# Kernel tuning notes

Hardware: AMD Instinct MI355X
Metric: run time of the kernel (lower is better)

## Reference

```python
import jax, jax.numpy as jnp
import numpy as np

B, T, N, F_IN, F_OUT = 8, 64, 256, 128, 64
NEG_INF = -9e15


def setup_inputs() -> dict:
    key = jax.random.key(0)
    k_h, k_w, k_a, k_adj = jax.random.split(key, 4)
    h = jax.random.normal(k_h, (B, T, N, F_IN), dtype=jnp.float32)
    W = jax.random.normal(k_w, (F_IN, F_OUT), dtype=jnp.float32) * (1.414 / np.sqrt(F_IN))
    a = jax.random.normal(k_a, (2 * F_OUT, 1), dtype=jnp.float32) * 0.1
    # binary adjacency with guaranteed self-loops so every softmax row is valid
    adj = (jax.random.uniform(k_adj, (N, N)) > 0.5).astype(jnp.float32)
    adj = jnp.maximum(adj, jnp.eye(N, dtype=jnp.float32))
    return {"h": h, "W": W, "a": a, "adj": adj}


def reference(h, W, a, adj):
    # Wh: [B, T, N, F_OUT]
    Wh = jnp.einsum('btnf,fo->btno', h, W)
    a1 = a[:F_OUT, 0]   # [F_OUT]
    a2 = a[F_OUT:, 0]   # [F_OUT]
    Wh1 = jnp.einsum('btno,o->btn', Wh, a1)  # source scores
    Wh2 = jnp.einsum('btno,o->btn', Wh, a2)  # target scores
    # e: [B, T, N, N] = leakyrelu(Wh1_i + Wh2_j)
    e = jax.nn.leaky_relu(Wh1[..., :, None] + Wh2[..., None, :], negative_slope=0.01)
    attention = jnp.where(adj > 0, e, NEG_INF)
    alpha = jax.nn.softmax(attention, axis=-1)
    # dropout is identity at inference (training=False)
    h_prime = jnp.einsum('btnm,btmo->btno', alpha, Wh)
    return jax.nn.elu(h_prime)  # concat=True path
```

## Files before the change

### kernel.cpp

```cpp
#include <hip/hip_runtime.h>
#include <hip/hip_bf16.h>

#define NN 256
#define FI 128
#define FO 64
#define LOG2E 1.4426950408889634f

typedef short s16x8 __attribute__((ext_vector_type(8)));
typedef float f32x4 __attribute__((ext_vector_type(4)));

__device__ __forceinline__ unsigned f2bf1(float x) {
  union { float f; unsigned u; } v; v.f = x;
  unsigned r = v.u + 0x7FFFu + ((v.u >> 16) & 1u);
  return r >> 16;
}
__device__ __forceinline__ unsigned pack2(float a, float b) {
  return f2bf1(a) | (f2bf1(b) << 16);
}
__device__ __forceinline__ unsigned pktrunc(float lo, float hi) {
  union { float f; unsigned u; } a, b; a.f = hi; b.f = lo;
  return __builtin_amdgcn_perm(a.u, b.u, 0x07060302u);
}
__device__ __forceinline__ float fexp2(float x) {
#if __has_builtin(__builtin_amdgcn_exp2f)
  return __builtin_amdgcn_exp2f(x);
#else
  return exp2f(x);
#endif
}

__device__ __forceinline__ void gload_lds16(const void* g, void* l) {
#if __has_builtin(__builtin_amdgcn_global_load_lds)
  __builtin_amdgcn_global_load_lds(
      (const __attribute__((address_space(1))) unsigned*)g,
      (__attribute__((address_space(3))) unsigned*)l, 16, 0, 0);
#else
  *(uint4*)l = *(const uint4*)g;
#endif
}

__global__ __launch_bounds__(256, 4)
void gat_wh(const float* __restrict__ h, const float* __restrict__ W,
            const float* __restrict__ a,
            unsigned short* __restrict__ whG,
            float* __restrict__ wh1G, float* __restrict__ wh2G)
{
  const int bid  = blockIdx.x;
  const int g    = bid >> 2;
  const int qt   = bid & 3;
  const int tid  = threadIdx.x;
  const int lane = tid & 63;
  const int w2   = tid >> 6;
  const int m    = lane & 15;
  const int q    = lane >> 4;
  const int R    = 64 * qt + 16 * w2;

  __shared__ __align__(16) unsigned short sWT[64 * 136];

  const float* __restrict__ hB = h + (size_t)g * NN * FI;

  float4 x[4][2];
  #pragma unroll
  for (int kt = 0; kt < 4; ++kt) {
    const float* p = hB + (size_t)(R + m) * FI + kt * 32 + q * 8;
    x[kt][0] = *(const float4*)p;
    x[kt][1] = *(const float4*)(p + 4);
  }

  #pragma unroll
  for (int it = 0; it < 4; ++it) {
    int idx = it * 256 + tid;
    int k   = (idx >> 4) << 1;
    int o   = (idx & 15) << 2;
    float4 wa = *(const float4*)&W[k * FO + o];
    float4 wb = *(const float4*)&W[(k + 1) * FO + o];
    *(unsigned*)&sWT[(o + 0) * 136 + k] = pack2(wa.x, wb.x);
    *(unsigned*)&sWT[(o + 1) * 136 + k] = pack2(wa.y, wb.y);
    *(unsigned*)&sWT[(o + 2) * 136 + k] = pack2(wa.z, wb.z);
    *(unsigned*)&sWT[(o + 3) * 136 + k] = pack2(wa.w, wb.w);
  }

  float a1v[4], a2v[4];
  #pragma unroll
  for (int nt = 0; nt < 4; ++nt) {
    a1v[nt] = a[16 * nt + m];
    a2v[nt] = a[FO + 16 * nt + m];
  }

  s16x8 af[4];
  #pragma unroll
  for (int kt = 0; kt < 4; ++kt) {
    union { unsigned u[4]; s16x8 v; } pk;
    pk.u[0] = pack2(x[kt][0].x, x[kt][0].y);
    pk.u[1] = pack2(x[kt][0].z, x[kt][0].w);
    pk.u[2] = pack2(x[kt][1].x, x[kt][1].y);
    pk.u[3] = pack2(x[kt][1].z, x[kt][1].w);
    af[kt] = pk.v;
  }

  __syncthreads();

  f32x4 acc[4];
  #pragma unroll
  for (int nt = 0; nt < 4; ++nt) acc[nt] = (f32x4){0.f, 0.f, 0.f, 0.f};
  #pragma unroll
  for (int kt = 0; kt < 4; ++kt)
    #pragma unroll
    for (int nt = 0; nt < 4; ++nt) {
      s16x8 bf = *(const s16x8*)&sWT[(16 * nt + m) * 136 + kt * 32 + q * 8];
      acc[nt] = __builtin_amdgcn_mfma_f32_16x16x32_bf16(af[kt], bf, acc[nt], 0, 0, 0);
    }

  {
    float p1[4] = {0.f,0.f,0.f,0.f}, p2[4] = {0.f,0.f,0.f,0.f};
    #pragma unroll
    for (int nt = 0; nt < 4; ++nt) {
      #pragma unroll
      for (int r = 0; r < 4; ++r) { p1[r] += acc[nt][r] * a1v[nt]; p2[r] += acc[nt][r] * a2v[nt]; }
    }
    #pragma unroll
    for (int off = 1; off < 16; off <<= 1)
      #pragma unroll
      for (int r = 0; r < 4; ++r) {
        p1[r] += __shfl_xor(p1[r], off);
        p2[r] += __shfl_xor(p2[r], off);
      }
    if (m == 0) {
      *(float4*)&wh1G[g * NN + R + 4 * q] =
          make_float4(p1[0]*LOG2E, p1[1]*LOG2E, p1[2]*LOG2E, p1[3]*LOG2E);
      *(float4*)&wh2G[g * NN + R + 4 * q] =
          make_float4(p2[0]*LOG2E, p2[1]*LOG2E, p2[2]*LOG2E, p2[3]*LOG2E);
    }
  }

  {
    const int Wv  = R >> 5;
    const int S   = (R >> 4) & 1;
    const int qB  = (2 * S + (q >> 1)) & 3;
    const int swz = (m & 3) ^ ((m >> 2) & 3);
    unsigned short* whP = whG + (size_t)g * (NN * FO);
    #pragma unroll
    for (int nt = 0; nt < 4; ++nt) {
      int chunk = ((Wv * 4 + nt) * 16 + m) * 4 + (qB ^ swz);
      uint2 wrv;
      wrv.x = pack2(acc[nt][0], acc[nt][1]);
      wrv.y = pack2(acc[nt][2], acc[nt][3]);
      *(uint2*)((char*)whP + chunk * 16 + (q & 1) * 8) = wrv;
    }
  }
}

__global__ __launch_bounds__(512)
__attribute__((amdgpu_waves_per_eu(4, 8)))
void gat_attn(const unsigned short* __restrict__ whG,
              const float* __restrict__ wh1G, const float* __restrict__ wh2G,
              const float* __restrict__ adj, float* __restrict__ out)
{
  const int bid  = blockIdx.x;
  const int g    = bid >> 1;
  const int hf   = bid & 1;
  const int tid  = threadIdx.x;
  const int lane = tid & 63;
  const int w2   = tid >> 6;
  const int m    = lane & 15;
  const int q    = lane >> 4;
  const int row  = 128 * hf + 16 * w2 + m;

  __shared__ __align__(16) unsigned short sWh[NN * FO];

  const unsigned short* __restrict__ whP = whG + (size_t)g * (NN * FO);
  const float* __restrict__ wh2B = wh2G + g * NN;
  const float* __restrict__ adjR = adj + (size_t)row * NN;

  #pragma unroll
  for (int i = 0; i < 4; ++i) {
    int c = i * 512 + tid;
    gload_lds16(whP + (size_t)c * 8, &sWh[(size_t)c * 8]);
  }

  const float w1 = wh1G[g * NN + row];

  s16x8 A[8];
  float sum = 0.f;
  #pragma unroll
  for (int kt = 0; kt < 8; ++kt) {
    if (kt) __builtin_amdgcn_sched_barrier(0x7);
    int j0 = kt * 32 + q * 8;
    float4 w20 = *(const float4*)&wh2B[j0];
    float4 w21 = *(const float4*)&wh2B[j0 + 4];
    float4 ad0 = *(const float4*)&adjR[j0];
    float4 ad1 = *(const float4*)&adjR[j0 + 4];
    float p[8];
    const float w2e[8] = {w20.x, w20.y, w20.z, w20.w, w21.x, w21.y, w21.z, w21.w};
    const float ade[8] = {ad0.x, ad0.y, ad0.z, ad0.w, ad1.x, ad1.y, ad1.z, ad1.w};
    #pragma unroll
    for (int e = 0; e < 8; ++e) {
      float l = w1 + w2e[e];
      l = fmaxf(l, 0.01f * l);
      float pe = fexp2(l) * ade[e];
      p[e] = pe;
      sum += pe;
    }
    union { unsigned u[4]; s16x8 v; } pk;
    pk.u[0] = pktrunc(p[0], p[1]);
    pk.u[1] = pktrunc(p[2], p[3]);
    pk.u[2] = pktrunc(p[4], p[5]);
    pk.u[3] = pktrunc(p[6], p[7]);
    A[kt] = pk.v;
  }
  sum += __shfl_xor(sum, 16);
  sum += __shfl_xor(sum, 32);
  const float inv = __builtin_amdgcn_rcpf(sum);

  __syncthreads();

  const int swz = (m & 3) ^ ((m >> 2) & 3);
  f32x4 acc[4];
  #pragma unroll
  for (int ot = 0; ot < 4; ++ot) acc[ot] = (f32x4){0.f, 0.f, 0.f, 0.f};
  #pragma unroll
  for (int kt = 0; kt < 8; ++kt) {
    #pragma unroll
    for (int ot = 0; ot < 4; ++ot) {
      int chunk = ((kt * 4 + ot) * 16 + m) * 4 + (q ^ swz);
      s16x8 whf = *(const s16x8*)&sWh[chunk * 8];
      acc[ot] = __builtin_amdgcn_mfma_f32_16x16x32_bf16(whf, A[kt], acc[ot], 0, 0, 0);
    }
  }

  float* outB = out + (size_t)g * NN * FO;
  #pragma unroll
  for (int ot = 0; ot < 4; ++ot) {
    float4 v4;
    float* vp = (float*)&v4;
    #pragma unroll
    for (int r = 0; r < 4; ++r) {
      float v = acc[ot][r] * inv;
      float ev = fexp2(v * LOG2E) - 1.f;
      vp[r] = v > 0.f ? v : ev;
    }
    *(float4*)&outB[row * FO + 16 * ot + 4 * q] = v4;
  }
}

extern "C" void kernel_launch(void* const* d_in, const int* in_sizes, int n_in,
                              void* d_out, int out_size, void* d_ws, size_t ws_size,
                              hipStream_t stream) {
  const float* h   = (const float*)d_in[0];
  const float* W   = (const float*)d_in[1];
  const float* a   = (const float*)d_in[2];
  const float* adj = (const float*)d_in[3];
  float* out = (float*)d_out;

  char* ws = (char*)d_ws;
  float*           wh1G = (float*)(ws);
  float*           wh2G = (float*)(ws + 524288);
  unsigned short*  whG  = (unsigned short*)(ws + 2 * 524288);

  gat_wh  <<<dim3(2048), dim3(256), 0, stream>>>(h, W, a, whG, wh1G, wh2G);
  gat_attn<<<dim3(1024), dim3(512), 0, stream>>>(whG, wh1G, wh2G, adj, out);
}
```

Baseline: 134.2 us.

## Compress adjacency to bitmask and process full graph per attention block

Adds a small kernel that ballots the float adjacency into a 256x256 bitmask, and the attention kernel now reads the bitmask instead of float adjacency rows, masking exp values with bit ops. Each attention block now handles all 256 rows of one graph (two row tiles per wave) instead of half, so the Wh tile is loaded into LDS once per graph rather than twice. This reduces adjacency and Wh traffic at the cost of an extra launch, half as many blocks, and more serial work per wave. The bitmask masking treats any adj>0 as 1 instead of multiplying by the adj value, which matches the reference for binary adjacency.

Measured after the change: 159.9 us. +19.2%, slower.

```diff
diff --git a/kernel.cpp b/kernel.cpp
--- a/kernel.cpp
+++ b/kernel.cpp
@@ -37,6 +37,18 @@
 #else
   *(uint4*)l = *(const uint4*)g;
 #endif
+}
+
+__global__ __launch_bounds__(256) void gat_k0(const float* __restrict__ adj,
+                                              unsigned* __restrict__ msk) {
+  const int row = blockIdx.x;
+  const int wv = threadIdx.x >> 6, lane = threadIdx.x & 63;
+  float v = adj[row * NN + wv * 64 + lane];
+  unsigned long long b = __ballot(v > 0.f);
+  if (lane == 0) {
+    msk[row * 8 + wv * 2]     = (unsigned)b;
+    msk[row * 8 + wv * 2 + 1] = (unsigned)(b >> 32);
+  }
 }
 
 __global__ __launch_bounds__(256, 4)
@@ -154,23 +166,20 @@
 __attribute__((amdgpu_waves_per_eu(4, 8)))
 void gat_attn(const unsigned short* __restrict__ whG,
               const float* __restrict__ wh1G, const float* __restrict__ wh2G,
-              const float* __restrict__ adj, float* __restrict__ out)
+              const unsigned* __restrict__ msk, float* __restrict__ out)
 {
-  const int bid  = blockIdx.x;
-  const int g    = bid >> 1;
-  const int hf   = bid & 1;
+  const int g    = blockIdx.x;
   const int tid  = threadIdx.x;
   const int lane = tid & 63;
   const int w2   = tid >> 6;
   const int m    = lane & 15;
   const int q    = lane >> 4;
-  const int row  = 128 * hf + 16 * w2 + m;
 
   __shared__ __align__(16) unsigned short sWh[NN * FO];
 
   const unsigned short* __restrict__ whP = whG + (size_t)g * (NN * FO);
   const float* __restrict__ wh2B = wh2G + g * NN;
-  const float* __restrict__ adjR = adj + (size_t)row * NN;
+  float* outB = out + (size_t)g * NN * FO;
 
   #pragma unroll
   for (int i = 0; i < 4; ++i) {
@@ -178,68 +187,74 @@
     gload_lds16(whP + (size_t)c * 8, &sWh[(size_t)c * 8]);
   }
 
-  const float w1 = wh1G[g * NN + row];
-
-  s16x8 A[8];
-  float sum = 0.f;
-  #pragma unroll
-  for (int kt = 0; kt < 8; ++kt) {
-    if (kt) __builtin_amdgcn_sched_barrier(0x7);
-    int j0 = kt * 32 + q * 8;
-    float4 w20 = *(const float4*)&wh2B[j0];
-    float4 w21 = *(const float4*)&wh2B[j0 + 4];
-    float4 ad0 = *(const float4*)&adjR[j0];
-    float4 ad1 = *(const float4*)&adjR[j0 + 4];
-    float p[8];
-    const float w2e[8] = {w20.x, w20.y, w20.z, w20.w, w21.x, w21.y, w21.z, w21.w};
-    const float ade[8] = {ad0.x, ad0.y, ad0.z, ad0.w, ad1.x, ad1.y, ad1.z, ad1.w};
-    #pragma unroll
-    for (int e = 0; e < 8; ++e) {
-      float l = w1 + w2e[e];
-      l = fmaxf(l, 0.01f * l);
-      float pe = fexp2(l) * ade[e];
-      p[e] = pe;
-      sum += pe;
-    }
-    union { unsigned u[4]; s16x8 v; } pk;
-    pk.u[0] = pktrunc(p[0], p[1]);
-    pk.u[1] = pktrunc(p[2], p[3]);
-    pk.u[2] = pktrunc(p[4], p[5]);
-    pk.u[3] = pktrunc(p[6], p[7]);
-    A[kt] = pk.v;
-  }
-  sum += __shfl_xor(sum, 16);
-  sum += __shfl_xor(sum, 32);
-  const float inv = __builtin_amdgcn_rcpf(sum);
-
-  __syncthreads();
-
   const int swz = (m & 3) ^ ((m >> 2) & 3);
-  f32x4 acc[4];
-  #pragma unroll
-  for (int ot = 0; ot < 4; ++ot) acc[ot] = (f32x4){0.f, 0.f, 0.f, 0.f};
-  #pragma unroll
-  for (int kt = 0; kt < 8; ++kt) {
+
+  #pragma unroll
+  for (int t = 0; t < 2; ++t) {
+    const int row = 32 * w2 + 16 * t + m;
+
+    const uint4 mka = *(const uint4*)&msk[row * 8];
+    const uint4 mkb = *(const uint4*)&msk[row * 8 + 4];
+    const unsigned mkw[8] = {mka.x, mka.y, mka.z, mka.w, mkb.x, mkb.y, mkb.z, mkb.w};
+    const float w1 = wh1G[g * NN + row];
+
+    s16x8 A[8];
+    float sum = 0.f;
+    #pragma unroll
+    for (int kt = 0; kt < 8; ++kt) {
+      int j0 = kt * 32 + q * 8;
+      float4 w20 = *(const float4*)&wh2B[j0];
+      float4 w21 = *(const float4*)&wh2B[j0 + 4];
+      unsigned wq = mkw[kt] >> (q * 8);
+      float p[8];
+      const float w2e[8] = {w20.x, w20.y, w20.z, w20.w, w21.x, w21.y, w21.z, w21.w};
+      #pragma unroll
+      for (int e = 0; e < 8; ++e) {
+        float l = w1 + w2e[e];
+        l = fmaxf(l, 0.01f * l);
+        union { float f; int i; } u_; u_.f = fexp2(l);
+        u_.i &= ((int)(wq << (31 - e))) >> 31;
+        p[e] = u_.f;
+        sum += u_.f;
+      }
+      union { unsigned u[4]; s16x8 v; } pk;
+      pk.u[0] = pktrunc(p[0], p[1]);
+      pk.u[1] = pktrunc(p[2], p[3]);
+      pk.u[2] = pktrunc(p[4], p[5]);
+      pk.u[3] = pktrunc(p[6], p[7]);
+      A[kt] = pk.v;
+    }
+    sum += __shfl_xor(sum, 16);
+    sum += __shfl_xor(sum, 32);
+    const float inv = __builtin_amdgcn_rcpf(sum);
+
+    if (t == 0) __syncthreads();
+
+    f32x4 acc[4];
+    #pragma unroll
+    for (int ot = 0; ot < 4; ++ot) acc[ot] = (f32x4){0.f, 0.f, 0.f, 0.f};
+    #pragma unroll
+    for (int kt = 0; kt < 8; ++kt) {
+      #pragma unroll
+      for (int ot = 0; ot < 4; ++ot) {
+        int chunk = ((kt * 4 + ot) * 16 + m) * 4 + (q ^ swz);
+        s16x8 whf = *(const s16x8*)&sWh[chunk * 8];
+        acc[ot] = __builtin_amdgcn_mfma_f32_16x16x32_bf16(whf, A[kt], acc[ot], 0, 0, 0);
+      }
+    }
+
     #pragma unroll
     for (int ot = 0; ot < 4; ++ot) {
-      int chunk = ((kt * 4 + ot) * 16 + m) * 4 + (q ^ swz);
-      s16x8 whf = *(const s16x8*)&sWh[chunk * 8];
-      acc[ot] = __builtin_amdgcn_mfma_f32_16x16x32_bf16(whf, A[kt], acc[ot], 0, 0, 0);
-    }
-  }
-
-  float* outB = out + (size_t)g * NN * FO;
-  #pragma unroll
-  for (int ot = 0; ot < 4; ++ot) {
-    float4 v4;
-    float* vp = (float*)&v4;
-    #pragma unroll
-    for (int r = 0; r < 4; ++r) {
-      float v = acc[ot][r] * inv;
-      float ev = fexp2(v * LOG2E) - 1.f;
-      vp[r] = v > 0.f ? v : ev;
-    }
-    *(float4*)&outB[row * FO + 16 * ot + 4 * q] = v4;
+      float4 v4;
+      float* vp = (float*)&v4;
+      #pragma unroll
+      for (int r = 0; r < 4; ++r) {
+        float v = acc[ot][r] * inv;
+        float ev = fexp2(v * LOG2E) - 1.f;
+        vp[r] = v > 0.f ? v : ev;
+      }
+      *(float4*)&outB[row * FO + 16 * ot + 4 * q] = v4;
+    }
   }
 }
 
@@ -253,10 +268,12 @@
   float* out = (float*)d_out;
 
   char* ws = (char*)d_ws;
-  float*           wh1G = (float*)(ws);
-  float*           wh2G = (float*)(ws + 524288);
-  unsigned short*  whG  = (unsigned short*)(ws + 2 * 524288);
-
+  unsigned*        msk  = (unsigned*)(ws);
+  float*           wh1G = (float*)(ws + 8192);
+  float*           wh2G = (float*)(ws + 8192 + 524288);
+  unsigned short*  whG  = (unsigned short*)(ws + 8192 + 2 * 524288);
+
+  gat_k0  <<<dim3(256),  dim3(256), 0, stream>>>(adj, msk);
   gat_wh  <<<dim3(2048), dim3(256), 0, stream>>>(h, W, a, whG, wh1G, wh2G);
-  gat_attn<<<dim3(1024), dim3(512), 0, stream>>>(whG, wh1G, wh2G, adj, out);
-}
+  gat_attn<<<dim3(512),  dim3(512), 0, stream>>>(whG, wh1G, wh2G, msk, out);
+}
```
